# Optimization experiments

Hardware: AMD Instinct MI355X
Metric: run time of the kernel (lower is better)

The kernel has to match this reference:

```python
import jax, jax.numpy as jnp
import numpy as np

B = 16384
TEXT_DIM = 768
IMAGE_DIM = 1024
HIDDEN = 1024
OUT_DIM = 1024
E = 8          # num_experts
K = 2          # top-k
NOISE_STD = 1.0
COMB = 2 * HIDDEN


def setup_inputs() -> dict:
    key = jax.random.key(0)
    ks = jax.random.split(key, 16)
    s = lambda d: 1.0 / np.sqrt(d)
    return {
        "text_emb": jax.random.normal(ks[0], (B, TEXT_DIM), jnp.float32),
        "image_emb": jax.random.normal(ks[1], (B, IMAGE_DIM), jnp.float32),
        "noise": jax.random.normal(ks[2], (B, E), jnp.float32),
        "Wt": jax.random.normal(ks[3], (TEXT_DIM, HIDDEN), jnp.float32) * s(TEXT_DIM),
        "bt": jnp.zeros((HIDDEN,), jnp.float32),
        "Wi": jax.random.normal(ks[4], (IMAGE_DIM, HIDDEN), jnp.float32) * s(IMAGE_DIM),
        "bi": jnp.zeros((HIDDEN,), jnp.float32),
        "Wg": jax.random.normal(ks[5], (COMB, E), jnp.float32) * s(COMB),
        "bg": jnp.zeros((E,), jnp.float32),
        "W1": jax.random.normal(ks[6], (E, COMB, HIDDEN), jnp.float32) * s(COMB),
        "b1": jnp.zeros((E, HIDDEN), jnp.float32),
        "W2": jax.random.normal(ks[7], (E, HIDDEN, OUT_DIM), jnp.float32) * s(HIDDEN),
        "b2": jnp.zeros((E, OUT_DIM), jnp.float32),
    }


def reference(text_emb, image_emb, noise, Wt, bt, Wi, bi, Wg, bg, W1, b1, W2, b2):
    # projections + concat -> combined [B, 2H]
    combined = jnp.concatenate([text_emb @ Wt + bt, image_emb @ Wi + bi], axis=-1)

    # noisy top-k gating
    clean_logits = combined @ Wg + bg            # [B, E]
    noisy_logits = clean_logits + noise * NOISE_STD
    topk_vals, topk_idx = jax.lax.top_k(noisy_logits, K)   # [B, K]
    topk_sm = jax.nn.softmax(topk_vals, axis=-1)
    rows = jnp.arange(combined.shape[0])[:, None]
    gate_weights = jnp.zeros_like(clean_logits).at[rows, topk_idx].set(topk_sm)  # [B, E]

    # run all experts densely (as in the original)
    h = jax.nn.relu(jnp.einsum('bd,edh->ebh', combined, W1) + b1[:, None, :])  # [E, B, H]
    out = jnp.einsum('ebh,eho->ebo', h, W2) + b2[:, None, :]                    # [E, B, O]

    # weighted sum over experts
    return jnp.einsum('be,ebo->bo', gate_weights, out)                          # [B, O]
```

## Files before the change

### kernel.cpp

```cpp
#include <hip/hip_runtime.h>
#include <stdint.h>
#include <stddef.h>

#define BB     16384
#define TD     768
#define ID_    1024
#define HID    1024
#define OD     1024
#define NE     8
#define CB     2048
#define CAPT   33792
#define GIN    1792

typedef __bf16 bf16;
typedef __bf16 bf16x4 __attribute__((ext_vector_type(4)));
typedef __bf16 bf16x8 __attribute__((ext_vector_type(8)));
typedef float  f32x4  __attribute__((ext_vector_type(4)));

struct Top2 { int e0, e1; float w0, w1; };
struct Slot2 { int p0, p1; };

__device__ __forceinline__ void gload16(void* lds, const void* g) {
#if __has_builtin(__builtin_amdgcn_global_load_lds)
  __builtin_amdgcn_global_load_lds(
      (const __attribute__((address_space(1))) void*)g,
      (__attribute__((address_space(3))) void*)lds, 16, 0, 0);
#else
  *(int4*)lds = *(const int4*)g;
#endif
}

__global__ void transpose_cvt(const float* __restrict__ src, bf16* __restrict__ dst,
                              int R, int C) {
  src += (size_t)blockIdx.z * R * C;
  dst += (size_t)blockIdx.z * R * C;
  __shared__ float tile[64][65];
  const int r0 = blockIdx.y * 64, c0 = blockIdx.x * 64;
  const int t = threadIdx.x;
#pragma unroll
  for (int i = 0; i < 16; ++i) {
    int e = i * 256 + t;
    int ii = e >> 6, jj = e & 63;
    tile[ii][jj] = src[(size_t)(r0 + ii) * C + (c0 + jj)];
  }
  __syncthreads();
#pragma unroll
  for (int i = 0; i < 16; ++i) {
    int e = i * 256 + t;
    int ii = e >> 6, jj = e & 63;
    dst[(size_t)(c0 + ii) * R + (r0 + jj)] = (bf16)tile[jj][ii];
  }
}

__global__ __launch_bounds__(256)
void fuse_w(const float* __restrict__ Wt, const float* __restrict__ Wi,
            const float* __restrict__ Wg, const float* __restrict__ bt,
            const float* __restrict__ bi, const float* __restrict__ bg,
            double* __restrict__ WgF, double* __restrict__ bgd) {
  const int o = blockIdx.x * 4 + (threadIdx.x >> 6);
  const int lane = threadIdx.x & 63;
  if (o >= (GIN + 1) * NE) return;
  const int idx = o >> 3, e = o & 7;
  double s = 0.0;
  if (idx < TD) {
    const float* wrow = Wt + (size_t)idx * HID;
    for (int h = lane; h < HID; h += 64)
      s += (double)wrow[h] * (double)Wg[(size_t)h * NE + e];
  } else if (idx < GIN) {
    const float* wrow = Wi + (size_t)(idx - TD) * HID;
    for (int h = lane; h < HID; h += 64)
      s += (double)wrow[h] * (double)Wg[(size_t)(HID + h) * NE + e];
  } else {
    for (int h = lane; h < HID; h += 64) {
      s += (double)bt[h] * (double)Wg[(size_t)h * NE + e];
      s += (double)bi[h] * (double)Wg[(size_t)(HID + h) * NE + e];
    }
  }
#pragma unroll
  for (int off = 32; off > 0; off >>= 1) s += __shfl_down(s, off);
  if (lane == 0) {
    if (idx < GIN) WgF[(size_t)e * GIN + idx] = s;
    else           bgd[e] = s + (double)bg[e];
  }
}

__global__ __launch_bounds__(1024)
void route1(const float* __restrict__ text, const float* __restrict__ image,
            const float* __restrict__ noise,
            const double* __restrict__ WgF, const double* __restrict__ bgd,
            bf16* __restrict__ text_b, bf16* __restrict__ image_b,
            Top2* __restrict__ top2, int* __restrict__ counts) {
  __shared__ double wg[NE * GIN];
  __shared__ int lcnt[NE];
  const int t = threadIdx.x;
  if (t < NE) lcnt[t] = 0;
  {
    const ulonglong2* src = (const ulonglong2*)WgF;
    ulonglong2* dst = (ulonglong2*)wg;
#pragma unroll
    for (int i = 0; i < (NE * GIN) / 2 / 1024; ++i)
      dst[i * 1024 + t] = src[i * 1024 + t];
  }
  __syncthreads();

  const int wave = t >> 6, lane = t & 63;
  const int row0 = blockIdx.x * 64;
#pragma unroll
  for (int rr = 0; rr < 4; ++rr) {
    const int row = row0 + wave + rr * 16;
    const float* tr = text + (size_t)row * TD;
    const float* ir = image + (size_t)row * ID_;
    float xv[28];
#pragma unroll
    for (int c = 0; c < 12; ++c) xv[c] = tr[lane + 64 * c];
#pragma unroll
    for (int c = 0; c < 16; ++c) xv[12 + c] = ir[lane + 64 * c];
    bf16* tb = text_b + (size_t)row * TD;
    bf16* ib = image_b + (size_t)row * ID_;
#pragma unroll
    for (int c = 0; c < 12; ++c) tb[lane + 64 * c] = (bf16)xv[c];
#pragma unroll
    for (int c = 0; c < 16; ++c) ib[lane + 64 * c] = (bf16)xv[12 + c];

    double acc[NE];
#pragma unroll
    for (int e = 0; e < NE; ++e) acc[e] = 0.0;
#pragma unroll
    for (int c = 0; c < 28; ++c) {
      const double vd = (double)xv[c];
      const int idx = lane + 64 * c;
#pragma unroll
      for (int e = 0; e < NE; ++e) acc[e] = fma(vd, wg[e * GIN + idx], acc[e]);
    }
#pragma unroll
    for (int off = 32; off > 0; off >>= 1) {
#pragma unroll
      for (int e = 0; e < NE; ++e) acc[e] += __shfl_down(acc[e], off);
    }
    if (lane == 0) {
      float nz[NE];
#pragma unroll
      for (int e = 0; e < NE; ++e)
        nz[e] = (float)(acc[e] + bgd[e]) + noise[(size_t)row * NE + e];
      int i0 = 0;
#pragma unroll
      for (int e = 1; e < NE; ++e) if (nz[e] > nz[i0]) i0 = e;
      int i1 = (i0 == 0) ? 1 : 0;
#pragma unroll
      for (int e = 0; e < NE; ++e) if (e != i0 && nz[e] > nz[i1]) i1 = e;
      float tt = expf(nz[i1] - nz[i0]);
      float w0 = 1.0f / (1.0f + tt);
      float w1 = tt / (1.0f + tt);
      Top2 rec; rec.e0 = i0; rec.e1 = i1; rec.w0 = w0; rec.w1 = w1;
      top2[row] = rec;
      atomicAdd(&lcnt[i0], 1);
      atomicAdd(&lcnt[i1], 1);
    }
  }
  __syncthreads();
  if (t < NE) atomicAdd(&counts[t], lcnt[t]);
}

__global__ void scan_pad(const int* __restrict__ counts, int* __restrict__ offsets,
                         int* __restrict__ padded, int* __restrict__ pos,
                         int* __restrict__ rows_list, float* __restrict__ wgt_list) {
  __shared__ int s_off[NE], s_cnt[NE], s_pad[NE];
  if (threadIdx.x == 0) {
    int off = 0;
    for (int e = 0; e < NE; ++e) {
      int c = counts[e];
      int pd = (c + 127) & ~127;
      s_cnt[e] = c; s_pad[e] = pd; s_off[e] = off;
      offsets[e] = off; padded[e] = pd; pos[e] = off;
      off += pd;
    }
    offsets[NE] = off;
  }
  __syncthreads();
  for (int e = 0; e < NE; ++e) {
    for (int i = s_cnt[e] + threadIdx.x; i < s_pad[e]; i += blockDim.x) {
      rows_list[s_off[e] + i] = 0;
      wgt_list[s_off[e] + i] = 0.0f;
    }
  }
}

__global__ void route2(const Top2* __restrict__ top2, int* __restrict__ pos,
                       int* __restrict__ rows_list, float* __restrict__ wgt_list,
                       Slot2* __restrict__ slots) {
  __shared__ int lcnt[NE], lbase[NE];
  if (threadIdx.x < NE) lcnt[threadIdx.x] = 0;
  __syncthreads();
  const int r = blockIdx.x * 256 + threadIdx.x;
  Top2 tt = top2[r];
  int s0 = atomicAdd(&lcnt[tt.e0], 1);
  int s1 = atomicAdd(&lcnt[tt.e1], 1);
  __syncthreads();
  if (threadIdx.x < NE)
    lbase[threadIdx.x] = atomicAdd(&pos[threadIdx.x], lcnt[threadIdx.x]);
  __syncthreads();
  int p0 = lbase[tt.e0] + s0;
  rows_list[p0] = r; wgt_list[p0] = tt.w0;
  int p1 = lbase[tt.e1] + s1;
  rows_list[p1] = r; wgt_list[p1] = tt.w1;
  Slot2 sl; sl.p0 = p0; sl.p1 = p1;
  slots[r] = sl;
}

__global__ __launch_bounds__(256)
void combine(const bf16* __restrict__ pairb, const Slot2* __restrict__ slots,
             float* __restrict__ out) {
  const int row = blockIdx.x;
  const Slot2 s = slots[row];
  const int t = threadIdx.x;
  const bf16x4 a = *(const bf16x4*)(pairb + (size_t)s.p0 * OD + t * 4);
  const bf16x4 b = *(const bf16x4*)(pairb + (size_t)s.p1 * OD + t * 4);
  f32x4 r;
#pragma unroll
  for (int j = 0; j < 4; ++j) r[j] = (float)a[j] + (float)b[j];
  *(f32x4*)(out + (size_t)row * OD + t * 4) = r;
}


#define BARe  do { __builtin_amdgcn_s_barrier(); __builtin_amdgcn_sched_barrier(0); } while (0)
#define VMC0  asm volatile("s_waitcnt vmcnt(0)" ::: "memory")
#define PRIO1 __builtin_amdgcn_s_setprio(1)
#define PRIO0 __builtin_amdgcn_s_setprio(0)

#define STAGE64(KT) do { \
  _Pragma("unroll") for (int j_ = 0; j_ < 4; ++j_) { \
    gload16(&As[ldso[j_]], aptr[j_] + (size_t)(KT) * 64); \
    gload16(&Bs[ldso[j_]], bptr[j_] + (size_t)(KT) * 64); \
  } \
} while (0)

template<int MODE>
__global__ __launch_bounds__(256, 4)
void gemm128(const bf16* __restrict__ A, const bf16* __restrict__ BT,
             const float* __restrict__ bias, bf16* __restrict__ outb,
             const int* __restrict__ rows_list, const float* __restrict__ wgt_list,
             const int* __restrict__ offsets, const int* __restrict__ padded,
             int K, int lda, int ldb, int ldout, int coloff) {
  __shared__ bf16 As[128 * 64];
  __shared__ bf16 Bs[128 * 64];
  const int t = threadIdx.x;
  const int lane = t & 63, w = t >> 6;
  const int wm = w >> 1, wn = w & 1;
  const int bid = blockIdx.x;
  const int xcd = bid & 7, sdec = bid >> 3;
  const int nblk = sdec & 7, mblk = (sdec >> 3) * 8 + xcd;

  long base = 0;
  if constexpr (MODE != 0) {
    const int e = blockIdx.z;
    if (mblk * 128 >= padded[e]) return;
    base = offsets[e];
    if constexpr (MODE == 1) { BT += (size_t)e * HID * CB; bias += e * HID; }
    else                     { BT += (size_t)e * OD * HID; bias += e * OD; }
  }

  const int scol = ((t & 7) ^ ((t >> 3) & 7)) * 8;
  const bf16* aptr[4]; const bf16* bptr[4]; int ldso[4];
#pragma unroll
  for (int j = 0; j < 4; ++j) {
    const int row = j * 32 + (t >> 3);
    long ga;
    if constexpr (MODE == 1)      ga = rows_list[base + (long)mblk * 128 + row];
    else if constexpr (MODE == 2) ga = base + (long)mblk * 128 + row;
    else                          ga = (long)mblk * 128 + row;
    aptr[j] = A + ga * lda + scol;
    bptr[j] = BT + (size_t)(nblk * 128 + row) * ldb + scol;
    ldso[j] = (j * 256 + t) * 8;
  }

  const int fr = lane & 15, hi = lane >> 4;
  const int rsw = hi ^ (fr & 7);
  int a_off[4], b_off[4];
#pragma unroll
  for (int f = 0; f < 4; ++f) {
    a_off[f] = ((wm * 64 + f * 16 + fr) * 8 + rsw) * 8;
    b_off[f] = ((wn * 64 + f * 16 + fr) * 8 + rsw) * 8;
  }

  f32x4 acc[4][4];
#pragma unroll
  for (int i = 0; i < 4; ++i)
#pragma unroll
    for (int j = 0; j < 4; ++j)
#pragma unroll
      for (int r = 0; r < 4; ++r) acc[i][j][r] = 0.0f;

  const int NKT = K >> 6;

  STAGE64(0);
  for (int kt = 0; kt < NKT; ++kt) {
    VMC0;
    BARe;
#pragma unroll
    for (int kk = 0; kk < 2; ++kk) {
      bf16x8 af[4], bfr[4];
#pragma unroll
      for (int f = 0; f < 4; ++f) af[f]  = *(const bf16x8*)(&As[a_off[f] ^ (kk * 32)]);
#pragma unroll
      for (int f = 0; f < 4; ++f) bfr[f] = *(const bf16x8*)(&Bs[b_off[f] ^ (kk * 32)]);
      PRIO1;
#pragma unroll
      for (int mf = 0; mf < 4; ++mf)
#pragma unroll
        for (int nf = 0; nf < 4; ++nf)
          acc[mf][nf] = __builtin_amdgcn_mfma_f32_16x16x32_bf16(af[mf], bfr[nf],
                                                                acc[mf][nf], 0, 0, 0);
      PRIO0;
    }
    BARe;
    if (kt + 1 < NKT) STAGE64(kt + 1);
  }

  const int row_h = hi * 4;
#pragma unroll
  for (int nf = 0; nf < 4; ++nf) {
    const int gcol = nblk * 128 + wn * 64 + nf * 16 + fr;
    const float bv = bias[gcol];
#pragma unroll
    for (int mf = 0; mf < 4; ++mf) {
      const int rbase = wm * 64 + mf * 16 + row_h;
#pragma unroll
      for (int r = 0; r < 4; ++r) {
        const int rit = rbase + r;
        float v = acc[mf][nf][r] + bv;
        if constexpr (MODE == 0) {
          outb[((size_t)mblk * 128 + rit) * ldout + coloff + gcol] = (bf16)v;
        } else if constexpr (MODE == 1) {
          outb[(size_t)(base + (long)mblk * 128 + rit) * ldout + gcol] =
              (bf16)fmaxf(v, 0.0f);
        } else {
          const long li = base + (long)mblk * 128 + rit;
          const float wgt = wgt_list[li];
          outb[(size_t)li * ldout + gcol] = (bf16)(wgt * v);
        }
      }
    }
  }
}

extern "C" void kernel_launch(void* const* d_in, const int* in_sizes, int n_in,
                              void* d_out, int out_size, void* d_ws, size_t ws_size,
                              hipStream_t stream) {
  const float* text  = (const float*)d_in[0];
  const float* image = (const float*)d_in[1];
  const float* noise = (const float*)d_in[2];
  const float* Wt    = (const float*)d_in[3];
  const float* bt    = (const float*)d_in[4];
  const float* Wi    = (const float*)d_in[5];
  const float* bi    = (const float*)d_in[6];
  const float* Wg    = (const float*)d_in[7];
  const float* bg    = (const float*)d_in[8];
  const float* W1    = (const float*)d_in[9];
  const float* b1    = (const float*)d_in[10];
  const float* W2    = (const float*)d_in[11];
  const float* b2    = (const float*)d_in[12];
  float* out = (float*)d_out;

  char* p = (char*)d_ws;
  auto alloc = [&](size_t bytes) {
    char* r = p; p += (bytes + 255) & ~(size_t)255; return r;
  };
  const size_t sz_text  = (size_t)BB * TD * 2;
  const size_t sz_texta = (sz_text + 255) & ~(size_t)255;
  const size_t sz_image = (size_t)BB * ID_ * 2;
  const size_t sz_pair  = (size_t)CAPT * OD * 2;
  size_t sz_u0 = sz_texta + sz_image;
  if (sz_pair > sz_u0) sz_u0 = sz_pair;
  char* u0 = alloc(sz_u0);
  bf16* text_b  = (bf16*)u0;
  bf16* image_b = (bf16*)(u0 + sz_texta);
  bf16* pairb   = (bf16*)u0;

  bf16*   WtT      = (bf16*)alloc((size_t)HID * TD * 2);
  bf16*   WiT      = (bf16*)alloc((size_t)HID * ID_ * 2);
  bf16*   W1T      = (bf16*)alloc((size_t)NE * HID * CB * 2);
  bf16*   W2T      = (bf16*)alloc((size_t)NE * OD * HID * 2);
  bf16*   combined = (bf16*)alloc((size_t)BB * CB * 2);
  bf16*   hbuf     = (bf16*)alloc((size_t)CAPT * HID * 2);
  double* WgF      = (double*)alloc((size_t)NE * GIN * 8);
  double* bgd      = (double*)alloc((size_t)NE * 8);
  Top2*   top2     = (Top2*)alloc((size_t)BB * sizeof(Top2));
  Slot2*  slots    = (Slot2*)alloc((size_t)BB * sizeof(Slot2));
  int*    counts   = (int*)alloc(NE * 4);
  int*    offsets  = (int*)alloc((NE + 1) * 4);
  int*    padded   = (int*)alloc(NE * 4);
  int*    pos      = (int*)alloc(NE * 4);
  int*    rows_list= (int*)alloc((size_t)CAPT * 4);
  float*  wgt_list = (float*)alloc((size_t)CAPT * 4);

  hipMemsetAsync(counts, 0, NE * 4, stream);

  transpose_cvt<<<dim3(HID / 64, TD / 64, 1),  256, 0, stream>>>(Wt, WtT, TD, HID);
  transpose_cvt<<<dim3(HID / 64, ID_ / 64, 1), 256, 0, stream>>>(Wi, WiT, ID_, HID);
  transpose_cvt<<<dim3(HID / 64, CB / 64, NE), 256, 0, stream>>>(W1, W1T, CB, HID);
  transpose_cvt<<<dim3(OD / 64, HID / 64, NE), 256, 0, stream>>>(W2, W2T, HID, OD);

  fuse_w<<<((GIN + 1) * NE + 3) / 4, 256, 0, stream>>>(
      Wt, Wi, Wg, bt, bi, bg, WgF, bgd);
  route1<<<BB / 64, 1024, 0, stream>>>(text, image, noise, WgF, bgd,
                                       text_b, image_b, top2, counts);
  scan_pad<<<1, 256, 0, stream>>>(counts, offsets, padded, pos, rows_list, wgt_list);
  route2<<<BB / 256, 256, 0, stream>>>(top2, pos, rows_list, wgt_list, slots);

  gemm128<0><<<dim3(1024, 1, 1), 256, 0, stream>>>(
      text_b, WtT, bt, combined, nullptr, nullptr, nullptr, nullptr,
      TD, TD, TD, CB, 0);
  gemm128<0><<<dim3(1024, 1, 1), 256, 0, stream>>>(
      image_b, WiT, bi, combined, nullptr, nullptr, nullptr, nullptr,
      ID_, ID_, ID_, CB, HID);
  gemm128<1><<<dim3(1024, 1, NE), 256, 0, stream>>>(
      combined, W1T, b1, hbuf, rows_list, nullptr, offsets, padded,
      CB, CB, CB, HID, 0);
  gemm128<2><<<dim3(1024, 1, NE), 256, 0, stream>>>(
      hbuf, W2T, b2, pairb, rows_list, wgt_list, offsets, padded,
      HID, HID, HID, OD, 0);
  combine<<<BB, 256, 0, stream>>>(pairb, slots, out);
}
```

Before: 504.8 us.

## Fold text/image projections into expert W1 weights to skip combined GEMMs

Precomputes per-expert effective weights W1eff = [Wt;Wi]·W1 (and an effective bias) with small GEMMs, so the expert first layer reads the bf16 text/image embeddings directly with K=1792 instead of first building the combined [B,2048] activations. This removes the two projection GEMMs over the full batch and the combined buffer traffic, and shrinks the expert-1 K dimension. In exchange it adds weight-side GEMMs on every call (8 experts × 1024×1792×1024) and a bias-folding kernel, and it changes rounding because the folded weights are stored in bf16.

```diff
diff --git a/kernel.cpp b/kernel.cpp
--- a/kernel.cpp
+++ b/kernel.cpp
@@ -50,6 +50,37 @@
     int ii = e >> 6, jj = e & 63;
     dst[(size_t)(c0 + ii) * R + (r0 + jj)] = (bf16)tile[jj][ii];
   }
+}
+
+__global__ __launch_bounds__(256)
+void cast_x(const float* __restrict__ Wt, const float* __restrict__ Wi,
+            bf16* __restrict__ Xb) {
+  const size_t i = ((size_t)blockIdx.x * 256 + threadIdx.x) * 8;
+  const float* s = (i < (size_t)TD * HID) ? (Wt + i) : (Wi + (i - (size_t)TD * HID));
+  f32x4 a = *(const f32x4*)s;
+  f32x4 b = *(const f32x4*)(s + 4);
+  bf16x8 o;
+#pragma unroll
+  for (int j = 0; j < 4; ++j) { o[j] = (bf16)a[j]; o[4 + j] = (bf16)b[j]; }
+  *(bf16x8*)(Xb + i) = o;
+}
+
+__global__ __launch_bounds__(256)
+void b1eff_k(const bf16* __restrict__ W1T, const float* __restrict__ bt,
+             const float* __restrict__ bi, const float* __restrict__ b1,
+             float* __restrict__ out) {
+  const int o = blockIdx.x * 256 + threadIdx.x;
+  const int e = o >> 10, n = o & 1023;
+  const bf16* wr = W1T + ((size_t)e * HID + n) * CB;
+  float s = b1[o];
+  for (int h8 = 0; h8 < HID / 8; ++h8) {
+    bf16x8 wa = *(const bf16x8*)(wr + h8 * 8);
+    bf16x8 wb = *(const bf16x8*)(wr + HID + h8 * 8);
+#pragma unroll
+    for (int j = 0; j < 8; ++j)
+      s += bt[h8 * 8 + j] * (float)wa[j] + bi[h8 * 8 + j] * (float)wb[j];
+  }
+  out[o] = s;
 }
 
 __global__ __launch_bounds__(256)
@@ -227,17 +258,11 @@
 #define PRIO1 __builtin_amdgcn_s_setprio(1)
 #define PRIO0 __builtin_amdgcn_s_setprio(0)
 
-#define STAGE64(KT) do { \
-  _Pragma("unroll") for (int j_ = 0; j_ < 4; ++j_) { \
-    gload16(&As[ldso[j_]], aptr[j_] + (size_t)(KT) * 64); \
-    gload16(&Bs[ldso[j_]], bptr[j_] + (size_t)(KT) * 64); \
-  } \
-} while (0)
-
 template<int MODE>
 __global__ __launch_bounds__(256, 4)
-void gemm128(const bf16* __restrict__ A, const bf16* __restrict__ BT,
-             const float* __restrict__ bias, bf16* __restrict__ outb,
+void gemm128(const bf16* __restrict__ A, const bf16* __restrict__ A2,
+             const bf16* __restrict__ BT, const float* __restrict__ bias,
+             bf16* __restrict__ outb,
              const int* __restrict__ rows_list, const float* __restrict__ wgt_list,
              const int* __restrict__ offsets, const int* __restrict__ padded,
              int K, int lda, int ldb, int ldout, int coloff) {
@@ -246,29 +271,45 @@
   const int t = threadIdx.x;
   const int lane = t & 63, w = t >> 6;
   const int wm = w >> 1, wn = w & 1;
-  const int bid = blockIdx.x;
-  const int xcd = bid & 7, sdec = bid >> 3;
-  const int nblk = sdec & 7, mblk = (sdec >> 3) * 8 + xcd;
+
+  int mblk, nblk;
+  if constexpr (MODE == 3) {
+    nblk = blockIdx.x; mblk = blockIdx.y;
+  } else {
+    const int bid = blockIdx.x;
+    const int xcd = bid & 7, sdec = bid >> 3;
+    nblk = sdec & 7; mblk = (sdec >> 3) * 8 + xcd;
+  }
 
   long base = 0;
-  if constexpr (MODE != 0) {
+  if constexpr (MODE == 1 || MODE == 2) {
     const int e = blockIdx.z;
     if (mblk * 128 >= padded[e]) return;
     base = offsets[e];
-    if constexpr (MODE == 1) { BT += (size_t)e * HID * CB; bias += e * HID; }
-    else                     { BT += (size_t)e * OD * HID; bias += e * OD; }
+    if constexpr (MODE == 1) { BT += (size_t)e * HID * GIN; bias += e * HID; }
+    else                     { BT += (size_t)e * OD * HID;  bias += e * OD; }
+  }
+  if constexpr (MODE == 3) {
+    const int e = blockIdx.z;
+    A += (size_t)e * HID * CB;
+    outb += (size_t)e * HID * GIN;
   }
 
   const int scol = ((t & 7) ^ ((t >> 3) & 7)) * 8;
-  const bf16* aptr[4]; const bf16* bptr[4]; int ldso[4];
+  const bf16* aptr[4]; const bf16* aptr2[4]; const bf16* bptr[4]; int ldso[4];
 #pragma unroll
   for (int j = 0; j < 4; ++j) {
     const int row = j * 32 + (t >> 3);
-    long ga;
-    if constexpr (MODE == 1)      ga = rows_list[base + (long)mblk * 128 + row];
-    else if constexpr (MODE == 2) ga = base + (long)mblk * 128 + row;
-    else                          ga = (long)mblk * 128 + row;
-    aptr[j] = A + ga * lda + scol;
+    if constexpr (MODE == 1) {
+      const long ga = rows_list[base + (long)mblk * 128 + row];
+      aptr[j]  = A  + ga * TD  + scol;
+      aptr2[j] = A2 + ga * ID_ + scol;
+    } else if constexpr (MODE == 2) {
+      const long ga = base + (long)mblk * 128 + row;
+      aptr[j] = A + ga * lda + scol;
+    } else {
+      aptr[j] = A + (size_t)(mblk * 128 + row) * lda + scol;
+    }
     bptr[j] = BT + (size_t)(nblk * 128 + row) * ldb + scol;
     ldso[j] = (j * 256 + t) * 8;
   }
@@ -292,7 +333,25 @@
 
   const int NKT = K >> 6;
 
-  STAGE64(0);
+  auto stage = [&](int kt) {
+    if constexpr (MODE == 1) {
+      if (kt < TD / 64) {
+#pragma unroll
+        for (int j = 0; j < 4; ++j) gload16(&As[ldso[j]], aptr[j] + (size_t)kt * 64);
+      } else {
+#pragma unroll
+        for (int j = 0; j < 4; ++j)
+          gload16(&As[ldso[j]], aptr2[j] + (size_t)(kt - TD / 64) * 64);
+      }
+    } else {
+#pragma unroll
+      for (int j = 0; j < 4; ++j) gload16(&As[ldso[j]], aptr[j] + (size_t)kt * 64);
+    }
+#pragma unroll
+    for (int j = 0; j < 4; ++j) gload16(&Bs[ldso[j]], bptr[j] + (size_t)kt * 64);
+  };
+
+  stage(0);
   for (int kt = 0; kt < NKT; ++kt) {
     VMC0;
     BARe;
@@ -313,14 +372,15 @@
       PRIO0;
     }
     BARe;
-    if (kt + 1 < NKT) STAGE64(kt + 1);
+    if (kt + 1 < NKT) stage(kt + 1);
   }
 
   const int row_h = hi * 4;
 #pragma unroll
   for (int nf = 0; nf < 4; ++nf) {
     const int gcol = nblk * 128 + wn * 64 + nf * 16 + fr;
-    const float bv = bias[gcol];
+    float bv = 0.0f;
+    if constexpr (MODE != 3) bv = bias[gcol];
 #pragma unroll
     for (int mf = 0; mf < 4; ++mf) {
       const int rbase = wm * 64 + mf * 16 + row_h;
@@ -328,15 +388,15 @@
       for (int r = 0; r < 4; ++r) {
         const int rit = rbase + r;
         float v = acc[mf][nf][r] + bv;
-        if constexpr (MODE == 0) {
-          outb[((size_t)mblk * 128 + rit) * ldout + coloff + gcol] = (bf16)v;
-        } else if constexpr (MODE == 1) {
+        if constexpr (MODE == 1) {
           outb[(size_t)(base + (long)mblk * 128 + rit) * ldout + gcol] =
               (bf16)fmaxf(v, 0.0f);
-        } else {
+        } else if constexpr (MODE == 2) {
           const long li = base + (long)mblk * 128 + rit;
           const float wgt = wgt_list[li];
           outb[(size_t)li * ldout + gcol] = (bf16)(wgt * v);
+        } else {
+          outb[((size_t)mblk * 128 + rit) * ldout + coloff + gcol] = (bf16)v;
         }
       }
     }
@@ -365,25 +425,24 @@
   auto alloc = [&](size_t bytes) {
     char* r = p; p += (bytes + 255) & ~(size_t)255; return r;
   };
-  const size_t sz_text  = (size_t)BB * TD * 2;
-  const size_t sz_texta = (sz_text + 255) & ~(size_t)255;
-  const size_t sz_image = (size_t)BB * ID_ * 2;
-  const size_t sz_pair  = (size_t)CAPT * OD * 2;
-  size_t sz_u0 = sz_texta + sz_image;
-  if (sz_pair > sz_u0) sz_u0 = sz_pair;
-  char* u0 = alloc(sz_u0);
-  bf16* text_b  = (bf16*)u0;
-  bf16* image_b = (bf16*)(u0 + sz_texta);
-  bf16* pairb   = (bf16*)u0;
-
-  bf16*   WtT      = (bf16*)alloc((size_t)HID * TD * 2);
-  bf16*   WiT      = (bf16*)alloc((size_t)HID * ID_ * 2);
-  bf16*   W1T      = (bf16*)alloc((size_t)NE * HID * CB * 2);
+
+  bf16* text_b  = (bf16*)alloc((size_t)BB * TD * 2);
+  bf16* image_b = (bf16*)alloc((size_t)BB * ID_ * 2);
+
+  const size_t sz_w1t  = (size_t)NE * HID * CB * 2;
+  const size_t sz_w1e  = (size_t)NE * HID * GIN * 2;
+  const size_t sz_pair = (size_t)CAPT * OD * 2;
+  char* u1 = alloc(sz_pair);
+  bf16* W1T    = (bf16*)u1;
+  bf16* W1effT = (bf16*)(u1 + sz_w1t);
+  bf16* Xb     = (bf16*)(u1 + sz_w1t + sz_w1e);
+  bf16* pairb  = (bf16*)u1;
+
   bf16*   W2T      = (bf16*)alloc((size_t)NE * OD * HID * 2);
-  bf16*   combined = (bf16*)alloc((size_t)BB * CB * 2);
   bf16*   hbuf     = (bf16*)alloc((size_t)CAPT * HID * 2);
   double* WgF      = (double*)alloc((size_t)NE * GIN * 8);
   double* bgd      = (double*)alloc((size_t)NE * 8);
+  float*  b1e      = (float*)alloc((size_t)NE * HID * 4);
   Top2*   top2     = (Top2*)alloc((size_t)BB * sizeof(Top2));
   Slot2*  slots    = (Slot2*)alloc((size_t)BB * sizeof(Slot2));
   int*    counts   = (int*)alloc(NE * 4);
@@ -395,29 +454,30 @@
 
   hipMemsetAsync(counts, 0, NE * 4, stream);
 
-  transpose_cvt<<<dim3(HID / 64, TD / 64, 1),  256, 0, stream>>>(Wt, WtT, TD, HID);
-  transpose_cvt<<<dim3(HID / 64, ID_ / 64, 1), 256, 0, stream>>>(Wi, WiT, ID_, HID);
   transpose_cvt<<<dim3(HID / 64, CB / 64, NE), 256, 0, stream>>>(W1, W1T, CB, HID);
   transpose_cvt<<<dim3(OD / 64, HID / 64, NE), 256, 0, stream>>>(W2, W2T, HID, OD);
+  cast_x<<<(GIN * HID) / 8 / 256, 256, 0, stream>>>(Wt, Wi, Xb);
 
   fuse_w<<<((GIN + 1) * NE + 3) / 4, 256, 0, stream>>>(
       Wt, Wi, Wg, bt, bi, bg, WgF, bgd);
+  b1eff_k<<<NE * HID / 256, 256, 0, stream>>>(W1T, bt, bi, b1, b1e);
   route1<<<BB / 64, 1024, 0, stream>>>(text, image, noise, WgF, bgd,
                                        text_b, image_b, top2, counts);
   scan_pad<<<1, 256, 0, stream>>>(counts, offsets, padded, pos, rows_list, wgt_list);
   route2<<<BB / 256, 256, 0, stream>>>(top2, pos, rows_list, wgt_list, slots);
 
-  gemm128<0><<<dim3(1024, 1, 1), 256, 0, stream>>>(
-      text_b, WtT, bt, combined, nullptr, nullptr, nullptr, nullptr,
-      TD, TD, TD, CB, 0);
-  gemm128<0><<<dim3(1024, 1, 1), 256, 0, stream>>>(
-      image_b, WiT, bi, combined, nullptr, nullptr, nullptr, nullptr,
-      ID_, ID_, ID_, CB, HID);
+  gemm128<3><<<dim3(TD / 128, HID / 128, NE), 256, 0, stream>>>(
+      W1T, nullptr, Xb, nullptr, W1effT, nullptr, nullptr, nullptr, nullptr,
+      HID, CB, HID, GIN, 0);
+  gemm128<3><<<dim3(ID_ / 128, HID / 128, NE), 256, 0, stream>>>(
+      W1T + HID, nullptr, Xb + (size_t)TD * HID, nullptr, W1effT,
+      nullptr, nullptr, nullptr, nullptr,
+      HID, CB, HID, GIN, TD);
   gemm128<1><<<dim3(1024, 1, NE), 256, 0, stream>>>(
-      combined, W1T, b1, hbuf, rows_list, nullptr, offsets, padded,
-      CB, CB, CB, HID, 0);
+      text_b, image_b, W1effT, b1e, hbuf, rows_list, nullptr, offsets, padded,
+      GIN, 0, GIN, HID, 0);
   gemm128<2><<<dim3(1024, 1, NE), 256, 0, stream>>>(
-      hbuf, W2T, b2, pairb, rows_list, wgt_list, offsets, padded,
+      hbuf, nullptr, W2T, b2, pairb, rows_list, wgt_list, offsets, padded,
       HID, HID, HID, OD, 0);
   combine<<<BB, 256, 0, stream>>>(pairb, slots, out);
 }
```

New measurement: 481.5 us. -4.6%, faster.
